# Performance work log

Measured on AMD Instinct MI355X. Metric: run time of the kernel, lower is better.

## Reference

```python
import jax, jax.numpy as jnp
import numpy as np

EPS = 1e-07


def setup_inputs() -> dict:
    key = jax.random.key(0)
    k1, k2, k3 = jax.random.split(key, 3)
    N, D, E = 100000, 128, 600000
    z = jax.random.normal(k1, (N, D), dtype=jnp.float32)
    edge_index = jax.random.randint(k2, (2, E), 0, N, dtype=jnp.int64)
    W = jax.random.normal(k3, (D,), dtype=jnp.float32) * (1.0 / np.sqrt(D))
    b = jnp.zeros((), dtype=jnp.float32)
    return {"z": z, "edge_index": edge_index, "W": W, "b": b}


def reference(z, edge_index, W, b):
    src = edge_index[0]
    dst = edge_index[1]
    z_i = z[src]                      # [E, D]
    z_j = z[dst]                      # [E, D]
    m_j = z_j @ W + b                 # [E]  (Linear(D,1).squeeze(-1))
    diff = z_i - z_j
    dist2 = jnp.sum(diff * diff, axis=-1) + EPS   # [E]
    log_d = jnp.log(dist2)
    logits = m_j - log_d
    prob = jax.nn.sigmoid(logits)
    return (logits, prob, m_j, dist2)
```

## Files before the change

### kernel.cpp

```cpp
#include <hip/hip_runtime.h>
#include <math.h>

#define D 128
#define EPS 1e-7f

typedef unsigned int uint;

__device__ __forceinline__ int sdot4(int a, int b, int c) {
#if __has_builtin(__builtin_amdgcn_sdot4)
    return __builtin_amdgcn_sdot4(a, b, c, false);
#else
    int r = c;
    #pragma unroll
    for (int i = 0; i < 4; ++i) {
        int av = (a << (24 - 8 * i)) >> 24;
        int bv = (b << (24 - 8 * i)) >> 24;
        r += av * bv;
    }
    return r;
#endif
}

__global__ __launch_bounds__(256) void node_precompute_kernel(
    const float* __restrict__ z, const float* __restrict__ W,
    const float* __restrict__ b,
    uint* __restrict__ zq,
    float4* __restrict__ meta, int N)
{
    const int lane = threadIdx.x & 63;
    const int half = lane >> 5, sub = lane & 31;
    const int n = (blockIdx.x * (blockDim.x >> 6) + (threadIdx.x >> 6)) * 2 + half;
    if (n >= N) return;

    const float4 a = ((const float4*)(z + (size_t)n * D))[sub];
    const float4 w = ((const float4*)W)[sub];

    float dot = a.x * w.x + a.y * w.y + a.z * w.z + a.w * w.w;
    float amax = fmaxf(fmaxf(fabsf(a.x), fabsf(a.y)), fmaxf(fabsf(a.z), fabsf(a.w)));
    #pragma unroll
    for (int off = 16; off > 0; off >>= 1) {
        dot  += __shfl_xor(dot, off);
        amax  = fmaxf(amax, __shfl_xor(amax, off));
    }

    const float s   = amax * (1.0f / 127.0f);
    const float inv = 127.0f / fmaxf(amax, 1e-30f);

    const int q0 = (int)rintf(fminf(fmaxf(a.x * inv, -127.f), 127.f));
    const int q1 = (int)rintf(fminf(fmaxf(a.y * inv, -127.f), 127.f));
    const int q2 = (int)rintf(fminf(fmaxf(a.z * inv, -127.f), 127.f));
    const int q3 = (int)rintf(fminf(fmaxf(a.w * inv, -127.f), 127.f));
    const uint pack = (uint)(q0 & 255) | ((uint)(q1 & 255) << 8)
                    | ((uint)(q2 & 255) << 16) | ((uint)q3 << 24);
    zq[(size_t)n * 32 + sub] = pack;

    int S = sdot4((int)pack, (int)pack, 0);
    #pragma unroll
    for (int off = 16; off > 0; off >>= 1) S += __shfl_xor(S, off);

    if (sub == 0) {
        float4 mt;
        mt.x = s;
        mt.y = (s * s) * (float)S;
        mt.z = dot + b[0];
        mt.w = 0.f;
        meta[n] = mt;
    }
}

__global__ __launch_bounds__(256) void edge_kernel(
    const uint* __restrict__ zq, const float4* __restrict__ meta,
    const int* __restrict__ ei, float* __restrict__ out, int E)
{
    const int lane = threadIdx.x & 63;
    const int sub = lane & 3;
    const int e = (blockIdx.x * (blockDim.x >> 6) + (threadIdx.x >> 6)) * 16
                  + (lane >> 2);
    if (e >= E) return;

    const int src = ei[e];
    const int dst = ei[E + e];

    const float4 Mi = meta[src];
    const float4 Mj = meta[dst];

    const uint4* ri = (const uint4*)(zq + (size_t)src * 32);
    const uint4* rj = (const uint4*)(zq + (size_t)dst * 32);
    const uint4 a0 = ri[sub];
    const uint4 a1 = ri[sub + 4];
    const uint4 c0 = rj[sub];
    const uint4 c1 = rj[sub + 4];

    int dot = sdot4((int)a0.x, (int)c0.x, 0);
    dot = sdot4((int)a0.y, (int)c0.y, dot);
    dot = sdot4((int)a0.z, (int)c0.z, dot);
    dot = sdot4((int)a0.w, (int)c0.w, dot);
    dot = sdot4((int)a1.x, (int)c1.x, dot);
    dot = sdot4((int)a1.y, (int)c1.y, dot);
    dot = sdot4((int)a1.z, (int)c1.z, dot);
    dot = sdot4((int)a1.w, (int)c1.w, dot);

    dot += __shfl_xor(dot, 1);
    dot += __shfl_xor(dot, 2);

    if (sub == 0) {
        const float wc = (Mi.x * Mj.x) * (float)dot;
        const float dist2 = fmaxf(Mi.y + Mj.y - wc - wc, 0.0f) + EPS;
        const float logits = Mj.z - __logf(dist2);
        const float prob   = 1.0f / (1.0f + __expf(-logits));
        out[e]         = logits;
        out[E + e]     = prob;
        out[2 * E + e] = Mj.z;
        out[3 * E + e] = dist2;
    }
}

__global__ __launch_bounds__(256) void gravity_decoder_fallback(
    const float* __restrict__ z, const int* __restrict__ ei,
    const float* __restrict__ W, const float* __restrict__ b,
    float* __restrict__ out, int E)
{
    const int lane = threadIdx.x & 63;
    const int half = lane >> 5, sub = lane & 31;
    const int e = (blockIdx.x * (blockDim.x >> 6) + (threadIdx.x >> 6)) * 2 + half;
    if (e >= E) return;
    const int src = ei[e], dst = ei[E + e];
    const float4* z4 = (const float4*)z;
    const float4 a = z4[(size_t)src * (D / 4) + sub];
    const float4 c = z4[(size_t)dst * (D / 4) + sub];
    const float4 w = ((const float4*)W)[sub];
    float dot = c.x * w.x + c.y * w.y + c.z * w.z + c.w * w.w;
    const float dx = a.x - c.x, dy = a.y - c.y, dz = a.z - c.z, dw = a.w - c.w;
    float d2 = dx * dx + dy * dy + dz * dz + dw * dw;
    #pragma unroll
    for (int off = 16; off > 0; off >>= 1) {
        dot += __shfl_xor(dot, off);
        d2  += __shfl_xor(d2,  off);
    }
    if (sub == 0) {
        const float mj = dot + b[0];
        const float dist2 = d2 + EPS;
        const float logits = mj - __logf(dist2);
        const float prob = 1.0f / (1.0f + __expf(-logits));
        out[e] = logits; out[E + e] = prob;
        out[2 * E + e] = mj; out[3 * E + e] = dist2;
    }
}

extern "C" void kernel_launch(void* const* d_in, const int* in_sizes, int n_in,
                              void* d_out, int out_size, void* d_ws, size_t ws_size,
                              hipStream_t stream)
{
    const float* z  = (const float*)d_in[0];
    const int*   ei = (const int*)d_in[1];
    const float* W  = (const float*)d_in[2];
    const float* b  = (const float*)d_in[3];
    float* out = (float*)d_out;

    const int E = in_sizes[1] / 2;
    const int N = in_sizes[0] / D;

    const size_t zq_bytes   = (size_t)N * D;
    const size_t meta_bytes = (size_t)N * sizeof(float4);

    if (ws_size >= zq_bytes + meta_bytes) {
        uint*   zq   = (uint*)d_ws;
        float4* meta = (float4*)((char*)d_ws + zq_bytes);

        const int nodes_per_block = 8;
        node_precompute_kernel<<<(N + nodes_per_block - 1) / nodes_per_block,
                                 256, 0, stream>>>(z, W, b, zq, meta, N);

        const int edges_per_block = 64;
        edge_kernel<<<(E + edges_per_block - 1) / edges_per_block,
                      256, 0, stream>>>(zq, meta, ei, out, E);
    } else {
        const int edges_per_block = 8;
        gravity_decoder_fallback<<<(E + edges_per_block - 1) / edges_per_block,
                                   256, 0, stream>>>(z, ei, W, b, out, E);
    }
}
```

Baseline: 117.7 us.

## Fuse node precompute and edge kernels into persistent kernel with grid barrier

Merges the node quantization kernel and the edge kernel into one persistent kernel with a fixed grid of 1024 blocks that uses grid-stride loops, separated by a software global barrier built on an atomic counter in workspace. The aim is to remove the second kernel launch and the gap between the two launches. In exchange it adds a memset launch, a spin-wait barrier that relies on all 1024 blocks being co-resident, and a fixed grid that may leave edge-phase parallelism underused.

```diff
diff --git a/kernel.cpp b/kernel.cpp
--- a/kernel.cpp
+++ b/kernel.cpp
@@ -21,97 +21,110 @@
 #endif
 }
 
-__global__ __launch_bounds__(256) void node_precompute_kernel(
+__global__ __launch_bounds__(256, 4) void fused_gravity(
     const float* __restrict__ z, const float* __restrict__ W,
-    const float* __restrict__ b,
-    uint* __restrict__ zq,
-    float4* __restrict__ meta, int N)
+    const float* __restrict__ b, const int* __restrict__ ei,
+    float* __restrict__ out, uint* __restrict__ zq,
+    float4* __restrict__ meta, uint* __restrict__ bar,
+    int N, int E, int nblocks)
 {
     const int lane = threadIdx.x & 63;
-    const int half = lane >> 5, sub = lane & 31;
-    const int n = (blockIdx.x * (blockDim.x >> 6) + (threadIdx.x >> 6)) * 2 + half;
-    if (n >= N) return;
+    const int wid  = blockIdx.x * (blockDim.x >> 6) + (threadIdx.x >> 6);
+    const int nw   = nblocks * (blockDim.x >> 6);
 
-    const float4 a = ((const float4*)(z + (size_t)n * D))[sub];
-    const float4 w = ((const float4*)W)[sub];
+    {
+        const int half = lane >> 5, sub = lane & 31;
+        const float4 w4 = ((const float4*)W)[sub];
+        const float bb = b[0];
+        for (int n = wid * 2 + half; n < N; n += nw * 2) {
+            const float4 a = ((const float4*)(z + (size_t)n * D))[sub];
 
-    float dot = a.x * w.x + a.y * w.y + a.z * w.z + a.w * w.w;
-    float amax = fmaxf(fmaxf(fabsf(a.x), fabsf(a.y)), fmaxf(fabsf(a.z), fabsf(a.w)));
-    #pragma unroll
-    for (int off = 16; off > 0; off >>= 1) {
-        dot  += __shfl_xor(dot, off);
-        amax  = fmaxf(amax, __shfl_xor(amax, off));
+            float dot = a.x * w4.x + a.y * w4.y + a.z * w4.z + a.w * w4.w;
+            float amax = fmaxf(fmaxf(fabsf(a.x), fabsf(a.y)),
+                               fmaxf(fabsf(a.z), fabsf(a.w)));
+            #pragma unroll
+            for (int off = 16; off > 0; off >>= 1) {
+                dot  += __shfl_xor(dot, off);
+                amax  = fmaxf(amax, __shfl_xor(amax, off));
+            }
+
+            const float s   = amax * (1.0f / 127.0f);
+            const float inv = 127.0f / fmaxf(amax, 1e-30f);
+
+            const int q0 = (int)rintf(fminf(fmaxf(a.x * inv, -127.f), 127.f));
+            const int q1 = (int)rintf(fminf(fmaxf(a.y * inv, -127.f), 127.f));
+            const int q2 = (int)rintf(fminf(fmaxf(a.z * inv, -127.f), 127.f));
+            const int q3 = (int)rintf(fminf(fmaxf(a.w * inv, -127.f), 127.f));
+            const uint pack = (uint)(q0 & 255) | ((uint)(q1 & 255) << 8)
+                            | ((uint)(q2 & 255) << 16) | ((uint)q3 << 24);
+            zq[(size_t)n * 32 + sub] = pack;
+
+            int S = sdot4((int)pack, (int)pack, 0);
+            #pragma unroll
+            for (int off = 16; off > 0; off >>= 1) S += __shfl_xor(S, off);
+
+            if (sub == 0) {
+                float4 mt;
+                mt.x = s;
+                mt.y = (s * s) * (float)S;
+                mt.z = dot + bb;
+                mt.w = 0.f;
+                meta[n] = mt;
+            }
+        }
     }
 
-    const float s   = amax * (1.0f / 127.0f);
-    const float inv = 127.0f / fmaxf(amax, 1e-30f);
+    __syncthreads();
+    if (threadIdx.x == 0) {
+        __threadfence();
+        __hip_atomic_fetch_add(bar, 1u, __ATOMIC_ACQ_REL, __HIP_MEMORY_SCOPE_AGENT);
+        while (__hip_atomic_load(bar, __ATOMIC_ACQUIRE, __HIP_MEMORY_SCOPE_AGENT)
+               < (uint)nblocks) {
+            __builtin_amdgcn_s_sleep(2);
+        }
+    }
+    __syncthreads();
 
-    const int q0 = (int)rintf(fminf(fmaxf(a.x * inv, -127.f), 127.f));
-    const int q1 = (int)rintf(fminf(fmaxf(a.y * inv, -127.f), 127.f));
-    const int q2 = (int)rintf(fminf(fmaxf(a.z * inv, -127.f), 127.f));
-    const int q3 = (int)rintf(fminf(fmaxf(a.w * inv, -127.f), 127.f));
-    const uint pack = (uint)(q0 & 255) | ((uint)(q1 & 255) << 8)
-                    | ((uint)(q2 & 255) << 16) | ((uint)q3 << 24);
-    zq[(size_t)n * 32 + sub] = pack;
+    {
+        const int sub = lane & 3;
+        const int g   = lane >> 2;
+        for (int e = wid * 16 + g; e < E; e += nw * 16) {
+            const int src = ei[e];
+            const int dst = ei[E + e];
 
-    int S = sdot4((int)pack, (int)pack, 0);
-    #pragma unroll
-    for (int off = 16; off > 0; off >>= 1) S += __shfl_xor(S, off);
+            const float4 Mi = meta[src];
+            const float4 Mj = meta[dst];
 
-    if (sub == 0) {
-        float4 mt;
-        mt.x = s;
-        mt.y = (s * s) * (float)S;
-        mt.z = dot + b[0];
-        mt.w = 0.f;
-        meta[n] = mt;
-    }
-}
+            const uint4* ri = (const uint4*)(zq + (size_t)src * 32);
+            const uint4* rj = (const uint4*)(zq + (size_t)dst * 32);
+            const uint4 a0 = ri[sub];
+            const uint4 a1 = ri[sub + 4];
+            const uint4 c0 = rj[sub];
+            const uint4 c1 = rj[sub + 4];
 
-__global__ __launch_bounds__(256) void edge_kernel(
-    const uint* __restrict__ zq, const float4* __restrict__ meta,
-    const int* __restrict__ ei, float* __restrict__ out, int E)
-{
-    const int lane = threadIdx.x & 63;
-    const int sub = lane & 3;
-    const int e = (blockIdx.x * (blockDim.x >> 6) + (threadIdx.x >> 6)) * 16
-                  + (lane >> 2);
-    if (e >= E) return;
+            int dot = sdot4((int)a0.x, (int)c0.x, 0);
+            dot = sdot4((int)a0.y, (int)c0.y, dot);
+            dot = sdot4((int)a0.z, (int)c0.z, dot);
+            dot = sdot4((int)a0.w, (int)c0.w, dot);
+            dot = sdot4((int)a1.x, (int)c1.x, dot);
+            dot = sdot4((int)a1.y, (int)c1.y, dot);
+            dot = sdot4((int)a1.z, (int)c1.z, dot);
+            dot = sdot4((int)a1.w, (int)c1.w, dot);
 
-    const int src = ei[e];
-    const int dst = ei[E + e];
+            dot += __shfl_xor(dot, 1);
+            dot += __shfl_xor(dot, 2);
 
-    const float4 Mi = meta[src];
-    const float4 Mj = meta[dst];
-
-    const uint4* ri = (const uint4*)(zq + (size_t)src * 32);
-    const uint4* rj = (const uint4*)(zq + (size_t)dst * 32);
-    const uint4 a0 = ri[sub];
-    const uint4 a1 = ri[sub + 4];
-    const uint4 c0 = rj[sub];
-    const uint4 c1 = rj[sub + 4];
-
-    int dot = sdot4((int)a0.x, (int)c0.x, 0);
-    dot = sdot4((int)a0.y, (int)c0.y, dot);
-    dot = sdot4((int)a0.z, (int)c0.z, dot);
-    dot = sdot4((int)a0.w, (int)c0.w, dot);
-    dot = sdot4((int)a1.x, (int)c1.x, dot);
-    dot = sdot4((int)a1.y, (int)c1.y, dot);
-    dot = sdot4((int)a1.z, (int)c1.z, dot);
-    dot = sdot4((int)a1.w, (int)c1.w, dot);
-
-    dot += __shfl_xor(dot, 1);
-    dot += __shfl_xor(dot, 2);
-
-    if (sub == 0) {
-        const float wc = (Mi.x * Mj.x) * (float)dot;
-        const float dist2 = fmaxf(Mi.y + Mj.y - wc - wc, 0.0f) + EPS;
-        const float logits = Mj.z - __logf(dist2);
-        const float prob   = 1.0f / (1.0f + __expf(-logits));
-        out[e]         = logits;
-        out[E + e]     = prob;
-        out[2 * E + e] = Mj.z;
-        out[3 * E + e] = dist2;
+            if (sub == 0) {
+                const float wc = (Mi.x * Mj.x) * (float)dot;
+                const float dist2 = fmaxf(Mi.y + Mj.y - wc - wc, 0.0f) + EPS;
+                const float logits = Mj.z - __logf(dist2);
+                const float prob   = 1.0f / (1.0f + __expf(-logits));
+                out[e]         = logits;
+                out[E + e]     = prob;
+                out[2 * E + e] = Mj.z;
+                out[3 * E + e] = dist2;
+            }
+        }
     }
 }
 
@@ -162,18 +175,18 @@
 
     const size_t zq_bytes   = (size_t)N * D;
     const size_t meta_bytes = (size_t)N * sizeof(float4);
+    const size_t bar_off    = zq_bytes + meta_bytes;
 
-    if (ws_size >= zq_bytes + meta_bytes) {
+    if (ws_size >= bar_off + 64) {
         uint*   zq   = (uint*)d_ws;
         float4* meta = (float4*)((char*)d_ws + zq_bytes);
+        uint*   bar  = (uint*)((char*)d_ws + bar_off);
 
-        const int nodes_per_block = 8;
-        node_precompute_kernel<<<(N + nodes_per_block - 1) / nodes_per_block,
-                                 256, 0, stream>>>(z, W, b, zq, meta, N);
+        hipMemsetAsync(bar, 0, sizeof(uint), stream);
 
-        const int edges_per_block = 64;
-        edge_kernel<<<(E + edges_per_block - 1) / edges_per_block,
-                      256, 0, stream>>>(zq, meta, ei, out, E);
+        const int grid = 1024;
+        fused_gravity<<<grid, 256, 0, stream>>>(z, W, b, ei, out, zq, meta, bar,
+                                                N, E, grid);
     } else {
         const int edges_per_block = 8;
         gravity_decoder_fallback<<<(E + edges_per_block - 1) / edges_per_block,
```

Measured after the change: 229.1 us. 94.6% more time.

## Remap edge kernel to 8 lanes per edge, two edges per lane group

Applied to the files above, without the earlier changes.

The edge kernel now assigns 8 lanes per edge, each loading a single uint4, and processes two edges per lane group. This raises memory-level parallelism by issuing four row loads per lane up front. All lanes now take part in the output stores, each writing one of the four outputs for one edge, instead of only one lane in four storing. The source meta is read as a float2, edge indices are clamped instead of returning early, and an occupancy hint of 8 is added to launch bounds. The cost is extra select logic and wider shuffle reductions.

```diff
diff --git a/kernel.cpp b/kernel.cpp
--- a/kernel.cpp
+++ b/kernel.cpp
@@ -68,51 +68,71 @@
     }
 }
 
-__global__ __launch_bounds__(256) void edge_kernel(
+__global__ __launch_bounds__(256, 8) void edge_kernel(
     const uint* __restrict__ zq, const float4* __restrict__ meta,
     const int* __restrict__ ei, float* __restrict__ out, int E)
 {
     const int lane = threadIdx.x & 63;
-    const int sub = lane & 3;
-    const int e = (blockIdx.x * (blockDim.x >> 6) + (threadIdx.x >> 6)) * 16
-                  + (lane >> 2);
-    if (e >= E) return;
-
-    const int src = ei[e];
-    const int dst = ei[E + e];
-
-    const float4 Mi = meta[src];
-    const float4 Mj = meta[dst];
-
-    const uint4* ri = (const uint4*)(zq + (size_t)src * 32);
-    const uint4* rj = (const uint4*)(zq + (size_t)dst * 32);
-    const uint4 a0 = ri[sub];
-    const uint4 a1 = ri[sub + 4];
-    const uint4 c0 = rj[sub];
-    const uint4 c1 = rj[sub + 4];
-
-    int dot = sdot4((int)a0.x, (int)c0.x, 0);
-    dot = sdot4((int)a0.y, (int)c0.y, dot);
-    dot = sdot4((int)a0.z, (int)c0.z, dot);
-    dot = sdot4((int)a0.w, (int)c0.w, dot);
-    dot = sdot4((int)a1.x, (int)c1.x, dot);
-    dot = sdot4((int)a1.y, (int)c1.y, dot);
-    dot = sdot4((int)a1.z, (int)c1.z, dot);
-    dot = sdot4((int)a1.w, (int)c1.w, dot);
-
-    dot += __shfl_xor(dot, 1);
-    dot += __shfl_xor(dot, 2);
-
-    if (sub == 0) {
-        const float wc = (Mi.x * Mj.x) * (float)dot;
-        const float dist2 = fmaxf(Mi.y + Mj.y - wc - wc, 0.0f) + EPS;
-        const float logits = Mj.z - __logf(dist2);
-        const float prob   = 1.0f / (1.0f + __expf(-logits));
-        out[e]         = logits;
-        out[E + e]     = prob;
-        out[2 * E + e] = Mj.z;
-        out[3 * E + e] = dist2;
-    }
+    const int sub8 = lane & 7;
+    const int grp  = lane >> 3;
+    const int wid  = blockIdx.x * (blockDim.x >> 6) + (threadIdx.x >> 6);
+    const int base = wid * 16;
+    const int m    = E - 1;
+
+    const int e0 = base + grp;
+    const int e1 = base + 8 + grp;
+    const int c0 = e0 <= m ? e0 : m;
+    const int c1 = e1 <= m ? e1 : m;
+
+    const int s0 = ei[c0], d0 = ei[E + c0];
+    const int s1 = ei[c1], d1 = ei[E + c1];
+
+    const uint4* zq4 = (const uint4*)zq;
+
+    const uint4 A0 = zq4[(size_t)s0 * 8 + sub8];
+    const uint4 B0 = zq4[(size_t)d0 * 8 + sub8];
+    const uint4 A1 = zq4[(size_t)s1 * 8 + sub8];
+    const uint4 B1 = zq4[(size_t)d1 * 8 + sub8];
+
+    const float2 Pi0 = *(const float2*)(meta + s0);
+    const float4 Pj0 = meta[d0];
+    const float2 Pi1 = *(const float2*)(meta + s1);
+    const float4 Pj1 = meta[d1];
+
+    int t0 = sdot4((int)A0.x, (int)B0.x, 0);
+    t0 = sdot4((int)A0.y, (int)B0.y, t0);
+    t0 = sdot4((int)A0.z, (int)B0.z, t0);
+    t0 = sdot4((int)A0.w, (int)B0.w, t0);
+
+    int t1 = sdot4((int)A1.x, (int)B1.x, 0);
+    t1 = sdot4((int)A1.y, (int)B1.y, t1);
+    t1 = sdot4((int)A1.z, (int)B1.z, t1);
+    t1 = sdot4((int)A1.w, (int)B1.w, t1);
+
+    t0 += __shfl_xor(t0, 1); t0 += __shfl_xor(t0, 2); t0 += __shfl_xor(t0, 4);
+    t1 += __shfl_xor(t1, 1); t1 += __shfl_xor(t1, 2); t1 += __shfl_xor(t1, 4);
+
+    const int sel = sub8 >> 2;
+    const int arr = sub8 & 3;
+
+    const float six = sel ? Pi1.x : Pi0.x;
+    const float siy = sel ? Pi1.y : Pi0.y;
+    const float sjx = sel ? Pj1.x : Pj0.x;
+    const float sjy = sel ? Pj1.y : Pj0.y;
+    const float sjz = sel ? Pj1.z : Pj0.z;
+    const int   td  = sel ? t1 : t0;
+    const int   ee  = sel ? e1 : e0;
+    const int   ce  = sel ? c1 : c0;
+
+    const float wc     = (six * sjx) * (float)td;
+    const float dist2  = fmaxf(siy + sjy - wc - wc, 0.0f) + EPS;
+    const float logits = sjz - __logf(dist2);
+    const float prob   = 1.0f / (1.0f + __expf(-logits));
+    const float val = (arr == 0) ? logits
+                    : (arr == 1) ? prob
+                    : (arr == 2) ? sjz : dist2;
+
+    if (ee <= m) out[(size_t)arr * E + ce] = val;
 }
 
 __global__ __launch_bounds__(256) void gravity_decoder_fallback(
```

Result: no change. 117.4 us (-0.2%).
